# Optimization experiments

Hardware: AMD Instinct MI355X
Metric: run time of the kernel (lower is better)

Reference implementation:

```python
import jax, jax.numpy as jnp
import numpy as np

DIM = 1024
HEADS = 16
DIM_HEAD = 64
INNER = HEADS * DIM_HEAD  # 1024
B, N = 2, 2048


def setup_inputs() -> dict:
    key = jax.random.key(0)
    ks = jax.random.split(key, 8)
    q = jax.random.normal(ks[0], (B, N, DIM), dtype=jnp.float32)
    k = jax.random.normal(ks[1], (B, N, DIM), dtype=jnp.float32)
    v = jax.random.normal(ks[2], (B, N, DIM), dtype=jnp.float32)
    # True = masked out (masked_fill semantics); causal mask broadcast over batch
    causal = jnp.triu(jnp.ones((N, N), dtype=jnp.bool_), k=1)
    mask = jnp.broadcast_to(causal, (B, N, N))
    s = 0.02
    Wq = jax.random.normal(ks[3], (DIM, INNER), dtype=jnp.float32) * s
    Wk = jax.random.normal(ks[4], (DIM, INNER), dtype=jnp.float32) * s
    Wv = jax.random.normal(ks[5], (DIM, INNER), dtype=jnp.float32) * s
    Wo = jax.random.normal(ks[6], (INNER, DIM), dtype=jnp.float32) * s
    bo = jnp.zeros((DIM,), dtype=jnp.float32)
    return {"q": q, "k": k, "v": v, "mask": mask,
            "Wq": Wq, "Wk": Wk, "Wv": Wv, "Wo": Wo, "bo": bo}


def reference(q, k, v, mask, Wq, Wk, Wv, Wo, bo):
    h, d = HEADS, DIM_HEAD
    scale = d ** -0.5
    b, n, _ = q.shape

    def heads_split(x):  # [b, n, h*d] -> [b, h, n, d]
        return x.reshape(b, -1, h, d).transpose(0, 2, 1, 3)

    qh = heads_split(q @ Wq)
    kh = heads_split(k @ Wk)
    vh = heads_split(v @ Wv)

    dots = jnp.einsum('bhid,bhjd->bhij', qh, kh) * scale  # [b,h,n,n]
    mask_value = -jnp.finfo(dots.dtype).max
    dots = jnp.where(mask[:, None, :, :], mask_value, dots)
    attn = jax.nn.softmax(dots, axis=-1)
    out = jnp.einsum('bhij,bhjd->bhid', attn, vh)          # [b,h,n,d]
    out = out.transpose(0, 2, 1, 3).reshape(b, n, h * d)    # [b,n,h*d]
    out = out @ Wo + bo                                     # RowParallelLinear (bias=True)
    return out  # dropout p=0.0 is identity
```

## Files before the change

kernel.cpp:

```cpp
#include <hip/hip_runtime.h>

typedef __attribute__((ext_vector_type(8))) short short8;
typedef __attribute__((ext_vector_type(4))) float f32x4;

#define MFMA_BF16(a, b, c) __builtin_amdgcn_mfma_f32_16x16x32_bf16((a), (b), (c), 0, 0, 0)

#define GLOAD16(g, l) __builtin_amdgcn_global_load_lds( \
    (const __attribute__((address_space(1))) void*)(g),  \
    (__attribute__((address_space(3))) void*)(l), 16, 0, 0)

#define BARRIER() __builtin_amdgcn_s_barrier()
#define LGKMCNT0() do { asm volatile("s_waitcnt lgkmcnt(0)" ::: "memory"); \
                        __builtin_amdgcn_sched_barrier(0); } while (0)
#define VMCNT(n) asm volatile("s_waitcnt vmcnt(" n ")" ::: "memory")

static __device__ __forceinline__ unsigned short f2bf(float f) {
    unsigned int u = __builtin_bit_cast(unsigned int, f);
    u += 0x7fffu + ((u >> 16) & 1u);
    return (unsigned short)(u >> 16);
}
static __device__ __forceinline__ unsigned int cvtpk(float a, float b) {
    unsigned int r;
    asm("v_cvt_pk_bf16_f32 %0, %1, %2" : "=v"(r) : "v"(a), "v"(b));
    return r;
}
static __device__ __forceinline__ float ex2(float x) {
    float r;
    asm("v_exp_f32 %0, %1" : "=v"(r) : "v"(x));
    return r;
}

__global__ __launch_bounds__(256) void convX_kernel(
    const float* __restrict__ q, const float* __restrict__ k, const float* __restrict__ v,
    unsigned short* __restrict__ dq, unsigned short* __restrict__ dk,
    unsigned short* __restrict__ dv)
{
    const float* s; unsigned short* d;
    switch (blockIdx.y) {
        case 0:  s = q; d = dq; break;
        case 1:  s = k; d = dk; break;
        default: s = v; d = dv; break;
    }
    int i = (blockIdx.x * 256 + threadIdx.x) * 8;
    float4 a = *reinterpret_cast<const float4*>(s + i);
    float4 b = *reinterpret_cast<const float4*>(s + i + 4);
    short8 o;
    o[0] = (short)f2bf(a.x); o[1] = (short)f2bf(a.y);
    o[2] = (short)f2bf(a.z); o[3] = (short)f2bf(a.w);
    o[4] = (short)f2bf(b.x); o[5] = (short)f2bf(b.y);
    o[6] = (short)f2bf(b.z); o[7] = (short)f2bf(b.w);
    *reinterpret_cast<short8*>(d + i) = o;
}

__global__ __launch_bounds__(256) void convWT_kernel(
    const float* __restrict__ w0, const float* __restrict__ w1,
    const float* __restrict__ w2, const float* __restrict__ w3,
    unsigned short* __restrict__ t0, unsigned short* __restrict__ t1,
    unsigned short* __restrict__ t2, unsigned short* __restrict__ t3)
{
    const float* W; unsigned short* T;
    switch (blockIdx.z) {
        case 0:  W = w0; T = t0; break;
        case 1:  W = w1; T = t1; break;
        case 2:  W = w2; T = t2; break;
        default: W = w3; T = t3; break;
    }
    __shared__ unsigned short ldsT[64][72];
    const int t = threadIdx.x;
    const int kb = blockIdx.x * 64, cb = blockIdx.y * 64;

    const int c4 = (t & 15) * 4;
    const int r0 = t >> 4;
    #pragma unroll
    for (int i = 0; i < 4; ++i) {
        int kr = r0 + i * 16;
        float4 wv = *reinterpret_cast<const float4*>(&W[(size_t)(kb + kr) * 1024 + cb + c4]);
        ldsT[c4 + 0][kr] = f2bf(wv.x);
        ldsT[c4 + 1][kr] = f2bf(wv.y);
        ldsT[c4 + 2][kr] = f2bf(wv.z);
        ldsT[c4 + 3][kr] = f2bf(wv.w);
    }
    __syncthreads();
    const int c = t >> 2;
    const int kp = (t & 3) * 16;
    short8 o0 = *reinterpret_cast<const short8*>(&ldsT[c][kp]);
    short8 o1 = *reinterpret_cast<const short8*>(&ldsT[c][kp + 8]);
    *reinterpret_cast<short8*>(&T[(size_t)(cb + c) * 1024 + kb + kp])     = o0;
    *reinterpret_cast<short8*>(&T[(size_t)(cb + c) * 1024 + kb + kp + 8]) = o1;
}

__device__ __forceinline__ void gemm_body(
    const unsigned short* __restrict__ A, const unsigned short* __restrict__ B,
    int tm, int cn, unsigned short* Al, unsigned short* Bl, f32x4 acc[4][4])
{
    const int t = threadIdx.x;
    const int lane = t & 63, w = t >> 6;
    const int lr = lane & 15, lg = lane >> 4;
    const int wr = w >> 1, wc = w & 1;

    const int srow = w * 16 + (lane >> 2);
    const int sk   = (lane & 3) * 8;
    const unsigned short* ga = A + (size_t)(tm + srow) * 1024 + sk;
    const unsigned short* gb = B + (size_t)(cn + srow) * 1024 + sk;
    unsigned short* la = Al + srow * 32 + sk;
    unsigned short* lb = Bl + srow * 32 + sk;

    for (int k0 = 0; k0 < 1024; k0 += 32) {
        __syncthreads();
        GLOAD16(ga + k0, la);
        GLOAD16(ga + k0 + (size_t)64 * 1024, la + 64 * 32);
        GLOAD16(gb + k0, lb);
        GLOAD16(gb + k0 + (size_t)64 * 1024, lb + 64 * 32);
        asm volatile("s_waitcnt vmcnt(0)" ::: "memory");
        __syncthreads();

        short8 af[4], bfr[4];
        #pragma unroll
        for (int i = 0; i < 4; ++i) {
            af[i]  = *reinterpret_cast<const short8*>(&Al[(wr * 64 + i * 16 + lr) * 32 + lg * 8]);
            bfr[i] = *reinterpret_cast<const short8*>(&Bl[(wc * 64 + i * 16 + lr) * 32 + lg * 8]);
        }
        #pragma unroll
        for (int mi = 0; mi < 4; ++mi)
            #pragma unroll
            for (int ni = 0; ni < 4; ++ni)
                acc[mi][ni] = MFMA_BF16(af[mi], bfr[ni], acc[mi][ni]);
    }
}

__global__ __launch_bounds__(512, 2) void qkv_gemm(
    const unsigned short* __restrict__ Xq, const unsigned short* __restrict__ Xk,
    const unsigned short* __restrict__ Xv,
    const unsigned short* __restrict__ WqT, const unsigned short* __restrict__ WkT,
    const unsigned short* __restrict__ WvT,
    unsigned short* __restrict__ Qh, unsigned short* __restrict__ Kh,
    unsigned short* __restrict__ VhT)
{
    extern __shared__ unsigned short lds[];
    const int t    = threadIdx.x;
    const int lane = t & 63, w = t >> 6;
    const int lr   = lane & 15, lg = lane >> 4;
    const int wrow = w >> 2, wcol = w & 3;
    const int sw   = lr & 7;

    const int z = blockIdx.z;
    const unsigned short *A, *B; unsigned short* dst;
    int tm, cn;
    if (z == 2)      { A = WvT; B = Xv;  dst = VhT; tm = blockIdx.y * 256; cn = blockIdx.x * 256; }
    else if (z == 1) { A = Xk;  B = WkT; dst = Kh;  tm = blockIdx.x * 256; cn = blockIdx.y * 256; }
    else             { A = Xq;  B = WqT; dst = Qh;  tm = blockIdx.x * 256; cn = blockIdx.y * 256; }

    const unsigned short* Ag = A + (size_t)tm * 1024;
    const unsigned short* Bg = B + (size_t)cn * 1024;

    const int sr    = t >> 3;
    const int gsw   = (t & 7) ^ (sr & 7);
    const int brow0 = (sr >> 5) * 64 + (sr & 31);

    auto stageA = [&](int q, int kt, unsigned short* slabA) {
        const unsigned short* g = Ag + (size_t)(q * 64 + sr) * 1024 + kt + gsw * 8;
        GLOAD16(g, slabA + q * 8192 + t * 8);
        GLOAD16(g + (size_t)128 * 1024, slabA + q * 8192 + 4096 + t * 8);
    };
    auto stageB = [&](int s, int kt, unsigned short* slabB) {
        const unsigned short* g = Bg + (size_t)(brow0 + s * 32) * 1024 + kt + gsw * 8;
        GLOAD16(g, slabB + s * 8192 + t * 8);
        GLOAD16(g + (size_t)128 * 1024, slabB + s * 8192 + 4096 + t * 8);
    };

    short8 rA[4][2], rB0[2][2], rB1[2][2];
    auto ldA = [&](const unsigned short* bufA, int q) {
        #pragma unroll
        for (int m2 = 0; m2 < 4; ++m2) {
            const unsigned short* p = bufA + q * 8192 + (wrow * 64 + m2 * 16 + lr) * 64;
            rA[m2][0] = *reinterpret_cast<const short8*>(p + (lg ^ sw) * 8);
            rA[m2][1] = *reinterpret_cast<const short8*>(p + ((4 + lg) ^ sw) * 8);
        }
    };
    auto ldB = [&](const unsigned short* bufB, int s, short8 rB[2][2]) {
        #pragma unroll
        for (int n2 = 0; n2 < 2; ++n2) {
            const unsigned short* p = bufB + s * 8192 + (wcol * 32 + n2 * 16 + lr) * 64;
            rB[n2][0] = *reinterpret_cast<const short8*>(p + (lg ^ sw) * 8);
            rB[n2][1] = *reinterpret_cast<const short8*>(p + ((4 + lg) ^ sw) * 8);
        }
    };

    f32x4 acc[8][4];
    #pragma unroll
    for (int i = 0; i < 8; ++i)
        #pragma unroll
        for (int j = 0; j < 4; ++j) acc[i][j] = (f32x4){0.f, 0.f, 0.f, 0.f};

#define QUAD(MH, NH, RB) do {                                            \
    _Pragma("unroll")                                                    \
    for (int m2 = 0; m2 < 4; ++m2) {                                     \
        _Pragma("unroll")                                                \
        for (int n2 = 0; n2 < 2; ++n2) {                                 \
            f32x4 c_ = acc[(MH)*4 + m2][(NH)*2 + n2];                    \
            c_ = MFMA_BF16(rA[m2][0], (RB)[n2][0], c_);                  \
            c_ = MFMA_BF16(rA[m2][1], (RB)[n2][1], c_);                  \
            acc[(MH)*4 + m2][(NH)*2 + n2] = c_;                          \
        } } } while (0)

    stageA(0, 0, lds);
    stageB(0, 0, lds + 16384);
    stageB(1, 0, lds + 16384);
    stageA(1, 0, lds);
    VMCNT("4");
    BARRIER();

    for (int tt = 0; tt < 15; ++tt) {
        unsigned short* cA = lds + (tt & 1) * 32768;
        unsigned short* cB = cA + 16384;
        unsigned short* nA = lds + ((tt + 1) & 1) * 32768;
        unsigned short* nB = nA + 16384;
        const int kn = (tt + 1) * 64;
        stageA(0, kn, nA);
        ldA(cA, 0); ldB(cB, 0, rB0);
        VMCNT("4"); BARRIER(); LGKMCNT0();
        __builtin_amdgcn_s_setprio(1); QUAD(0, 0, rB0); __builtin_amdgcn_s_setprio(0);
        BARRIER();
        stageB(0, kn, nB);
        ldB(cB, 1, rB1);
        VMCNT("4"); BARRIER(); LGKMCNT0();
        __builtin_amdgcn_s_setprio(1); QUAD(0, 1, rB1); __builtin_amdgcn_s_setprio(0);
        BARRIER();
        stageB(1, kn, nB);
        ldA(cA, 1);
        BARRIER(); LGKMCNT0();
        __builtin_amdgcn_s_setprio(1); QUAD(1, 1, rB1); __builtin_amdgcn_s_setprio(0);
        BARRIER();
        stageA(1, kn, nA);
        VMCNT("4"); BARRIER(); LGKMCNT0();
        __builtin_amdgcn_s_setprio(1); QUAD(1, 0, rB0); __builtin_amdgcn_s_setprio(0);
        BARRIER();
    }
    {
        unsigned short* cA = lds + 32768;
        unsigned short* cB = cA + 16384;
        ldA(cA, 0); ldB(cB, 0, rB0);
        VMCNT("2"); BARRIER(); LGKMCNT0();
        __builtin_amdgcn_s_setprio(1); QUAD(0, 0, rB0); __builtin_amdgcn_s_setprio(0);
        BARRIER();
        ldB(cB, 1, rB1);
        VMCNT("0"); BARRIER(); LGKMCNT0();
        __builtin_amdgcn_s_setprio(1); QUAD(0, 1, rB1); __builtin_amdgcn_s_setprio(0);
        BARRIER();
        ldA(cA, 1);
        LGKMCNT0();
        __builtin_amdgcn_s_setprio(1); QUAD(1, 1, rB1); QUAD(1, 0, rB0);
        __builtin_amdgcn_s_setprio(0);
    }
#undef QUAD

    if (z == 2) {
        #pragma unroll
        for (int mi = 0; mi < 8; ++mi)
            #pragma unroll
            for (int ni = 0; ni < 4; ++ni)
                #pragma unroll
                for (int r = 0; r < 4; ++r) {
                    int c    = tm + wrow * 128 + mi * 16 + lg * 4 + r;
                    int nseq = cn + wcol * 64 + ni * 16 + lr;
                    int b = nseq >> 11, n = nseq & 2047;
                    int h = c >> 6, d = c & 63;
                    dst[(((size_t)(b * 16 + h) * 64 + d) << 11) + n] = f2bf(acc[mi][ni][r]);
                }
    } else {
        const float sc = (z == 0) ? 0.18033688011112042f : 1.0f;
        #pragma unroll
        for (int mi = 0; mi < 8; ++mi)
            #pragma unroll
            for (int ni = 0; ni < 4; ++ni)
                #pragma unroll
                for (int r = 0; r < 4; ++r) {
                    int orow = tm + wrow * 128 + mi * 16 + lg * 4 + r;
                    int ocol = cn + wcol * 64 + ni * 16 + lr;
                    int b = orow >> 11, n = orow & 2047;
                    int h = ocol >> 6, d = ocol & 63;
                    dst[(((size_t)(b * 16 + h) * 2048 + n) << 6) + d] = f2bf(acc[mi][ni][r] * sc);
                }
    }
}

__global__ __launch_bounds__(256) void o_gemm(
    const unsigned short* __restrict__ Ctx, const unsigned short* __restrict__ WoT,
    const float* __restrict__ bias, float* __restrict__ out)
{
    __shared__ unsigned short Al[128 * 32];
    __shared__ unsigned short Bl[128 * 32];
    const int tm = blockIdx.x * 128, cn = blockIdx.y * 128;

    f32x4 acc[4][4];
    #pragma unroll
    for (int i = 0; i < 4; ++i)
        #pragma unroll
        for (int j = 0; j < 4; ++j) acc[i][j] = (f32x4){0.f, 0.f, 0.f, 0.f};

    gemm_body(Ctx, WoT, tm, cn, Al, Bl, acc);

    const int lane = threadIdx.x & 63, w = threadIdx.x >> 6;
    const int lr = lane & 15, lg = lane >> 4;
    const int wr = w >> 1, wc = w & 1;

    #pragma unroll
    for (int mi = 0; mi < 4; ++mi)
        #pragma unroll
        for (int ni = 0; ni < 4; ++ni)
            #pragma unroll
            for (int r = 0; r < 4; ++r) {
                int orow = tm + wr * 64 + mi * 16 + lg * 4 + r;
                int ocol = cn + wc * 64 + ni * 16 + lr;
                out[(size_t)orow * 1024 + ocol] = acc[mi][ni][r] + bias[ocol];
            }
}

__global__ __launch_bounds__(256, 2) void attn_kernel(
    const unsigned short* __restrict__ Qh, const unsigned short* __restrict__ Kh,
    const unsigned short* __restrict__ VhT, unsigned short* __restrict__ Ctx)
{
    __shared__ unsigned short KV[2][8192];
    __shared__ unsigned int PlT[4][16][20];

    const int t  = threadIdx.x;
    const int l  = t & 63, w = t >> 6;
    const int lr = l & 15, lg = l >> 4;
    const int rg = w & 1, jh = w >> 1;
    const int swz = lr & 7;

    const int lin  = blockIdx.x;
    const int xcd  = lin & 7;
    const int j    = lin >> 3;
    const int bh   = xcd * 4 + (j & 3);
    const int u    = j >> 2;
    const int strip = (u & 1) ? (u >> 1) : (31 - (u >> 1));
    const int b    = bh >> 4, h = bh & 15;

    const unsigned short* Qb = Qh  + (size_t)bh * (2048 * 64);
    const unsigned short* Kb = Kh  + (size_t)bh * (2048 * 64);
    const unsigned short* Vb = VhT + (size_t)bh * (64 * 2048);

    const int srow = t >> 3;
    const int sg   = (t & 7) ^ (srow & 7);

    auto stage = [&](int jt, int bf) {
        const unsigned short* kg0 = Kb + (size_t)(jt + srow) * 64 + sg * 8;
        unsigned short* kl = &KV[bf][0] + w * 512;
        GLOAD16(kg0, kl);
        GLOAD16(kg0 + 32 * 64, kl + 2048);
        const unsigned short* vg0 = Vb + (size_t)srow * 2048 + jt + sg * 8;
        unsigned short* vl = &KV[bf][4096] + w * 512;
        GLOAD16(vg0, vl);
        GLOAD16(vg0 + (size_t)32 * 2048, vl + 2048);
    };

    const int qbase = strip * 64 + rg * 32;
    const int ns    = strip + 1;

    short8 bQ[2][2];
    #pragma unroll
    for (int qg = 0; qg < 2; ++qg) {
        const unsigned short* qp = Qb + (size_t)(qbase + qg * 16 + lr) * 64 + lg * 8;
        bQ[qg][0] = *reinterpret_cast<const short8*>(qp);
        bQ[qg][1] = *reinterpret_cast<const short8*>(qp + 32);
    }

    f32x4 acc[2][4];
    #pragma unroll
    for (int qg = 0; qg < 2; ++qg)
        #pragma unroll
        for (int di = 0; di < 4; ++di) acc[qg][di] = (f32x4){0.f, 0.f, 0.f, 0.f};
    float lsum[2] = {0.f, 0.f};

    stage(0, 0);
    __syncthreads();

    for (int s = 0; s < ns; ++s) {
        const int buf = s & 1;
        if (s + 1 < ns) stage(64 * (s + 1), buf ^ 1);

        const int jt = 64 * s + jh * 32;
        const unsigned short* Ks = &KV[buf][0];
        const unsigned short* Vs = &KV[buf][4096];

        short8 aK[2][2];
        #pragma unroll
        for (int kg = 0; kg < 2; ++kg) {
            const int rT = jh * 32 + kg * 16 + lr;
            aK[kg][0] = *reinterpret_cast<const short8*>(Ks + rT * 64 + ((lg ^ swz) << 3));
            aK[kg][1] = *reinterpret_cast<const short8*>(Ks + rT * 64 + (((4 + lg) ^ swz) << 3));
        }
        short8 bV[4];
        #pragma unroll
        for (int di = 0; di < 4; ++di) {
            const int d = lr + 16 * di;
            bV[di] = *reinterpret_cast<const short8*>(Vs + d * 64 + (((jh * 4 + lg) ^ swz) << 3));
        }

        f32x4 sf[2][2];
        #pragma unroll
        for (int kg = 0; kg < 2; ++kg)
            #pragma unroll
            for (int qg = 0; qg < 2; ++qg) {
                f32x4 z = (f32x4){0.f, 0.f, 0.f, 0.f};
                z = MFMA_BF16(aK[kg][0], bQ[qg][0], z);
                sf[kg][qg] = MFMA_BF16(aK[kg][1], bQ[qg][1], z);
            }

        #pragma unroll
        for (int qg = 0; qg < 2; ++qg) {
            const int qrow = qbase + qg * 16 + lr;
            float p[8];
            if (jt + 31 > qbase + qg * 16) {
                #pragma unroll
                for (int r = 0; r < 4; ++r) {
                    p[r]     = (jt + lg * 4 + r      > qrow) ? 0.f : ex2(sf[0][qg][r]);
                    p[4 + r] = (jt + 16 + lg * 4 + r > qrow) ? 0.f : ex2(sf[1][qg][r]);
                }
            } else {
                #pragma unroll
                for (int r = 0; r < 4; ++r) {
                    p[r] = ex2(sf[0][qg][r]); p[4 + r] = ex2(sf[1][qg][r]);
                }
            }

            float ps = (p[0] + p[1]) + (p[2] + p[3]) + (p[4] + p[5]) + (p[6] + p[7]);
            ps += __shfl_xor(ps, 16);
            ps += __shfl_xor(ps, 32);
            lsum[qg] += ps;

            PlT[w][lr][lg * 2]         = cvtpk(p[0], p[1]);
            PlT[w][lr][lg * 2 + 1]     = cvtpk(p[2], p[3]);
            PlT[w][lr][8 + lg * 2]     = cvtpk(p[4], p[5]);
            PlT[w][lr][8 + lg * 2 + 1] = cvtpk(p[6], p[7]);

            short8 aP = *reinterpret_cast<const short8*>(&PlT[w][lr][lg * 4]);
            #pragma unroll
            for (int di = 0; di < 4; ++di)
                acc[qg][di] = MFMA_BF16(aP, bV[di], acc[qg][di]);
        }
        __syncthreads();
    }

    float* cmb = (float*)&KV[0][0];
    if (jh == 1) {
        float* cp = cmb + (size_t)(rg * 64 + l) * 36;
        #pragma unroll
        for (int qg = 0; qg < 2; ++qg)
            #pragma unroll
            for (int di = 0; di < 4; ++di)
                *reinterpret_cast<f32x4*>(cp + (qg * 4 + di) * 4) = acc[qg][di];
        cp[32] = lsum[0]; cp[33] = lsum[1];
    }
    __syncthreads();
    if (jh == 0) {
        const float* cp = cmb + (size_t)(rg * 64 + l) * 36;
        #pragma unroll
        for (int qg = 0; qg < 2; ++qg) {
            #pragma unroll
            for (int di = 0; di < 4; ++di)
                acc[qg][di] += *reinterpret_cast<const f32x4*>(cp + (qg * 4 + di) * 4);
            float lt = lsum[qg] + cp[32 + qg];
            float linv[4];
            #pragma unroll
            for (int r = 0; r < 4; ++r) linv[r] = 1.f / __shfl(lt, lg * 4 + r);
            #pragma unroll
            for (int di = 0; di < 4; ++di) {
                #pragma unroll
                for (int r = 0; r < 4; ++r) {
                    int row = qbase + qg * 16 + lg * 4 + r;
                    Ctx[(size_t)(b * 2048 + row) * 1024 + h * 64 + di * 16 + lr] =
                        f2bf(acc[qg][di][r] * linv[r]);
                }
            }
        }
    }
}

extern "C" void kernel_launch(void* const* d_in, const int* in_sizes, int n_in,
                              void* d_out, int out_size, void* d_ws, size_t ws_size,
                              hipStream_t stream) {
    const float* q  = (const float*)d_in[0];
    const float* k  = (const float*)d_in[1];
    const float* v  = (const float*)d_in[2];
    const float* Wq = (const float*)d_in[4];
    const float* Wk = (const float*)d_in[5];
    const float* Wv = (const float*)d_in[6];
    const float* Wo = (const float*)d_in[7];
    const float* bo = (const float*)d_in[8];
    float* out = (float*)d_out;

    const size_t HSZ = (size_t)32 * 2048 * 64;
    const size_t WSZ = (size_t)1024 * 1024;
    unsigned short* Qh  = (unsigned short*)d_ws;
    unsigned short* Kh  = Qh + HSZ;
    unsigned short* VhT = Kh + HSZ;
    unsigned short* Xqb = VhT + HSZ;
    unsigned short* Xkb = Xqb + HSZ;
    unsigned short* Xvb = Xkb + HSZ;
    unsigned short* WqT = Xvb + HSZ;
    unsigned short* WkT = WqT + WSZ;
    unsigned short* WvT = WkT + WSZ;
    unsigned short* WoT = WvT + WSZ;
    unsigned short* Ctx = Xqb;

    hipFuncSetAttribute(reinterpret_cast<const void*>(qkv_gemm),
                        hipFuncAttributeMaxDynamicSharedMemorySize, 131072);

    dim3 blk(256);
    convX_kernel<<<dim3(2048, 3), blk, 0, stream>>>(q, k, v, Xqb, Xkb, Xvb);
    convWT_kernel<<<dim3(16, 16, 4), blk, 0, stream>>>(Wq, Wk, Wv, Wo, WqT, WkT, WvT, WoT);
    qkv_gemm<<<dim3(16, 4, 3), dim3(512), 131072, stream>>>(Xqb, Xkb, Xvb, WqT, WkT, WvT, Qh, Kh, VhT);
    attn_kernel<<<dim3(1024), blk, 0, stream>>>(Qh, Kh, VhT, Ctx);
    o_gemm<<<dim3(32, 8), blk, 0, stream>>>(Ctx, WoT, bo, out);
}
```

Before: 118.4 us.

## Restructure attention into 512-thread blocks processing paired causal strips

The attention kernel now launches 512 blocks of 512 threads, each handling a pair of query strips (pidx and 31-pidx) in two passes to balance causal work. Each wave owns 16 query rows instead of 32. V fragments are now read directly from global memory into registers instead of being staged in LDS, leaving only K double-buffered in shared memory. This aims to improve occupancy and load balance and cut LDS traffic, at the cost of uncoalesced strided global V reads and extra barriers between passes.

```diff
diff --git a/kernel.cpp b/kernel.cpp
--- a/kernel.cpp
+++ b/kernel.cpp
@@ -316,25 +316,26 @@
             }
 }
 
-__global__ __launch_bounds__(256, 2) void attn_kernel(
+__global__ __launch_bounds__(512, 4) void attn_kernel(
     const unsigned short* __restrict__ Qh, const unsigned short* __restrict__ Kh,
     const unsigned short* __restrict__ VhT, unsigned short* __restrict__ Ctx)
 {
-    __shared__ unsigned short KV[2][8192];
-    __shared__ unsigned int PlT[4][16][20];
+    __shared__ unsigned char SH[26624];
+    unsigned short* KL  = (unsigned short*)SH;
+    unsigned int* PlT   = (unsigned int*)(SH + 16384);
+    float* cmb          = (float*)SH;
 
     const int t  = threadIdx.x;
     const int l  = t & 63, w = t >> 6;
     const int lr = l & 15, lg = l >> 4;
-    const int rg = w & 1, jh = w >> 1;
+    const int rg = w >> 1, jh = w & 1;
     const int swz = lr & 7;
 
     const int lin  = blockIdx.x;
     const int xcd  = lin & 7;
-    const int j    = lin >> 3;
-    const int bh   = xcd * 4 + (j & 3);
-    const int u    = j >> 2;
-    const int strip = (u & 1) ? (u >> 1) : (31 - (u >> 1));
+    const int idx  = lin >> 3;
+    const int bh   = xcd * 4 + (idx >> 4);
+    const int pidx = idx & 15;
     const int b    = bh >> 4, h = bh & 15;
 
     const unsigned short* Qb = Qh  + (size_t)bh * (2048 * 64);
@@ -344,124 +345,110 @@
     const int srow = t >> 3;
     const int sg   = (t & 7) ^ (srow & 7);
 
-    auto stage = [&](int jt, int bf) {
+    auto stageK = [&](int jt, int bf) {
         const unsigned short* kg0 = Kb + (size_t)(jt + srow) * 64 + sg * 8;
-        unsigned short* kl = &KV[bf][0] + w * 512;
-        GLOAD16(kg0, kl);
-        GLOAD16(kg0 + 32 * 64, kl + 2048);
-        const unsigned short* vg0 = Vb + (size_t)srow * 2048 + jt + sg * 8;
-        unsigned short* vl = &KV[bf][4096] + w * 512;
-        GLOAD16(vg0, vl);
-        GLOAD16(vg0 + (size_t)32 * 2048, vl + 2048);
+        GLOAD16(kg0, KL + bf * 4096 + w * 512);
     };
 
-    const int qbase = strip * 64 + rg * 32;
-    const int ns    = strip + 1;
-
-    short8 bQ[2][2];
-    #pragma unroll
-    for (int qg = 0; qg < 2; ++qg) {
-        const unsigned short* qp = Qb + (size_t)(qbase + qg * 16 + lr) * 64 + lg * 8;
-        bQ[qg][0] = *reinterpret_cast<const short8*>(qp);
-        bQ[qg][1] = *reinterpret_cast<const short8*>(qp + 32);
-    }
-
-    f32x4 acc[2][4];
-    #pragma unroll
-    for (int qg = 0; qg < 2; ++qg)
-        #pragma unroll
-        for (int di = 0; di < 4; ++di) acc[qg][di] = (f32x4){0.f, 0.f, 0.f, 0.f};
-    float lsum[2] = {0.f, 0.f};
-
-    stage(0, 0);
-    __syncthreads();
-
-    for (int s = 0; s < ns; ++s) {
-        const int buf = s & 1;
-        if (s + 1 < ns) stage(64 * (s + 1), buf ^ 1);
-
-        const int jt = 64 * s + jh * 32;
-        const unsigned short* Ks = &KV[buf][0];
-        const unsigned short* Vs = &KV[buf][4096];
-
-        short8 aK[2][2];
-        #pragma unroll
-        for (int kg = 0; kg < 2; ++kg) {
-            const int rT = jh * 32 + kg * 16 + lr;
-            aK[kg][0] = *reinterpret_cast<const short8*>(Ks + rT * 64 + ((lg ^ swz) << 3));
-            aK[kg][1] = *reinterpret_cast<const short8*>(Ks + rT * 64 + (((4 + lg) ^ swz) << 3));
-        }
-        short8 bV[4];
-        #pragma unroll
-        for (int di = 0; di < 4; ++di) {
-            const int d = lr + 16 * di;
-            bV[di] = *reinterpret_cast<const short8*>(Vs + d * 64 + (((jh * 4 + lg) ^ swz) << 3));
-        }
-
-        f32x4 sf[2][2];
-        #pragma unroll
-        for (int kg = 0; kg < 2; ++kg)
-            #pragma unroll
-            for (int qg = 0; qg < 2; ++qg) {
+    #pragma unroll 1
+    for (int pass = 0; pass < 2; ++pass) {
+        const int strip = pass ? (31 - pidx) : pidx;
+        const int qbase = strip * 64 + rg * 16;
+        const int ns    = strip + 1;
+
+        short8 bQ[2];
+        {
+            const unsigned short* qp = Qb + (size_t)(qbase + lr) * 64 + lg * 8;
+            bQ[0] = *reinterpret_cast<const short8*>(qp);
+            bQ[1] = *reinterpret_cast<const short8*>(qp + 32);
+        }
+
+        f32x4 acc[4];
+        #pragma unroll
+        for (int di = 0; di < 4; ++di) acc[di] = (f32x4){0.f, 0.f, 0.f, 0.f};
+        float lsum = 0.f;
+
+        if (pass) __syncthreads();
+        stageK(0, 0);
+        __syncthreads();
+
+        for (int s = 0; s < ns; ++s) {
+            const int buf = s & 1;
+            const int jt = 64 * s + jh * 32;
+
+            short8 bV[4];
+            {
+                const unsigned short* vp = Vb + jt + lg * 8;
+                #pragma unroll
+                for (int di = 0; di < 4; ++di)
+                    bV[di] = *reinterpret_cast<const short8*>(vp + (size_t)(lr + 16 * di) * 2048);
+            }
+
+            if (s + 1 < ns) stageK(64 * (s + 1), buf ^ 1);
+
+            const unsigned short* Ks = KL + buf * 4096;
+            short8 aK[2][2];
+            #pragma unroll
+            for (int kg = 0; kg < 2; ++kg) {
+                const int rT = jh * 32 + kg * 16 + lr;
+                aK[kg][0] = *reinterpret_cast<const short8*>(Ks + rT * 64 + ((lg ^ swz) << 3));
+                aK[kg][1] = *reinterpret_cast<const short8*>(Ks + rT * 64 + (((4 + lg) ^ swz) << 3));
+            }
+
+            f32x4 sf[2];
+            #pragma unroll
+            for (int kg = 0; kg < 2; ++kg) {
                 f32x4 z = (f32x4){0.f, 0.f, 0.f, 0.f};
-                z = MFMA_BF16(aK[kg][0], bQ[qg][0], z);
-                sf[kg][qg] = MFMA_BF16(aK[kg][1], bQ[qg][1], z);
+                z = MFMA_BF16(aK[kg][0], bQ[0], z);
+                sf[kg] = MFMA_BF16(aK[kg][1], bQ[1], z);
             }
 
-        #pragma unroll
-        for (int qg = 0; qg < 2; ++qg) {
-            const int qrow = qbase + qg * 16 + lr;
+            const int qrow = qbase + lr;
             float p[8];
-            if (jt + 31 > qbase + qg * 16) {
+            if (jt + 31 > qbase) {
                 #pragma unroll
                 for (int r = 0; r < 4; ++r) {
-                    p[r]     = (jt + lg * 4 + r      > qrow) ? 0.f : ex2(sf[0][qg][r]);
-                    p[4 + r] = (jt + 16 + lg * 4 + r > qrow) ? 0.f : ex2(sf[1][qg][r]);
+                    p[r]     = (jt + lg * 4 + r      > qrow) ? 0.f : ex2(sf[0][r]);
+                    p[4 + r] = (jt + 16 + lg * 4 + r > qrow) ? 0.f : ex2(sf[1][r]);
                 }
             } else {
                 #pragma unroll
-                for (int r = 0; r < 4; ++r) {
-                    p[r] = ex2(sf[0][qg][r]); p[4 + r] = ex2(sf[1][qg][r]);
-                }
+                for (int r = 0; r < 4; ++r) { p[r] = ex2(sf[0][r]); p[4 + r] = ex2(sf[1][r]); }
             }
 
             float ps = (p[0] + p[1]) + (p[2] + p[3]) + (p[4] + p[5]) + (p[6] + p[7]);
             ps += __shfl_xor(ps, 16);
             ps += __shfl_xor(ps, 32);
-            lsum[qg] += ps;
-
-            PlT[w][lr][lg * 2]         = cvtpk(p[0], p[1]);
-            PlT[w][lr][lg * 2 + 1]     = cvtpk(p[2], p[3]);
-            PlT[w][lr][8 + lg * 2]     = cvtpk(p[4], p[5]);
-            PlT[w][lr][8 + lg * 2 + 1] = cvtpk(p[6], p[7]);
-
-            short8 aP = *reinterpret_cast<const short8*>(&PlT[w][lr][lg * 4]);
+            lsum += ps;
+
+            unsigned int* pr = PlT + (w * 16 + lr) * 20;
+            pr[lg * 2]         = cvtpk(p[0], p[1]);
+            pr[lg * 2 + 1]     = cvtpk(p[2], p[3]);
+            pr[8 + lg * 2]     = cvtpk(p[4], p[5]);
+            pr[8 + lg * 2 + 1] = cvtpk(p[6], p[7]);
+
+            short8 aP = *reinterpret_cast<const short8*>(pr + lg * 4);
             #pragma unroll
             for (int di = 0; di < 4; ++di)
-                acc[qg][di] = MFMA_BF16(aP, bV[di], acc[qg][di]);
+                acc[di] = MFMA_BF16(aP, bV[di], acc[di]);
+
+            __syncthreads();
+        }
+
+        if (jh == 1) {
+            float* cp = cmb + (size_t)(rg * 64 + l) * 20;
+            #pragma unroll
+            for (int di = 0; di < 4; ++di)
+                *reinterpret_cast<f32x4*>(cp + di * 4) = acc[di];
+            cp[16] = lsum;
         }
         __syncthreads();
-    }
-
-    float* cmb = (float*)&KV[0][0];
-    if (jh == 1) {
-        float* cp = cmb + (size_t)(rg * 64 + l) * 36;
-        #pragma unroll
-        for (int qg = 0; qg < 2; ++qg)
+        if (jh == 0) {
+            const float* cp = cmb + (size_t)(rg * 64 + l) * 20;
             #pragma unroll
             for (int di = 0; di < 4; ++di)
-                *reinterpret_cast<f32x4*>(cp + (qg * 4 + di) * 4) = acc[qg][di];
-        cp[32] = lsum[0]; cp[33] = lsum[1];
-    }
-    __syncthreads();
-    if (jh == 0) {
-        const float* cp = cmb + (size_t)(rg * 64 + l) * 36;
-        #pragma unroll
-        for (int qg = 0; qg < 2; ++qg) {
-            #pragma unroll
-            for (int di = 0; di < 4; ++di)
-                acc[qg][di] += *reinterpret_cast<const f32x4*>(cp + (qg * 4 + di) * 4);
-            float lt = lsum[qg] + cp[32 + qg];
+                acc[di] += *reinterpret_cast<const f32x4*>(cp + di * 4);
+            float lt = lsum + cp[16];
             float linv[4];
             #pragma unroll
             for (int r = 0; r < 4; ++r) linv[r] = 1.f / __shfl(lt, lg * 4 + r);
@@ -469,9 +456,9 @@
             for (int di = 0; di < 4; ++di) {
                 #pragma unroll
                 for (int r = 0; r < 4; ++r) {
-                    int row = qbase + qg * 16 + lg * 4 + r;
+                    int row = qbase + lg * 4 + r;
                     Ctx[(size_t)(b * 2048 + row) * 1024 + h * 64 + di * 16 + lr] =
-                        f2bf(acc[qg][di][r] * linv[r]);
+                        f2bf(acc[di][r] * linv[r]);
                 }
             }
         }
@@ -512,6 +499,6 @@
     convX_kernel<<<dim3(2048, 3), blk, 0, stream>>>(q, k, v, Xqb, Xkb, Xvb);
     convWT_kernel<<<dim3(16, 16, 4), blk, 0, stream>>>(Wq, Wk, Wv, Wo, WqT, WkT, WvT, WoT);
     qkv_gemm<<<dim3(16, 4, 3), dim3(512), 131072, stream>>>(Xqb, Xkb, Xvb, WqT, WkT, WvT, Qh, Kh, VhT);
-    attn_kernel<<<dim3(1024), blk, 0, stream>>>(Qh, Kh, VhT, Ctx);
+    attn_kernel<<<dim3(512), dim3(512), 0, stream>>>(Qh, Kh, VhT, Ctx);
     o_gemm<<<dim3(32, 8), blk, 0, stream>>>(Ctx, WoT, bo, out);
 }
```

Result: slower. 142.7 us (+20.5%).
